# Optimization experiments

Measured on AMD Instinct MI355X. Metric: run time of the kernel, lower is better.

Reference implementation:

```python
import jax, jax.numpy as jnp
import numpy as np

C = 512
H = 8
P = 64
B = 4
N = 1024


def setup_inputs() -> dict:
    key = jax.random.key(0)
    ks = jax.random.split(key, 12)
    s = 0.02
    return {
        "tokens": jax.random.normal(ks[0], (B, N, C), dtype=jnp.float32),
        "pair_features": jax.random.normal(ks[1], (N, N, P), dtype=jnp.float32),
        "Wq": jax.random.normal(ks[2], (C, C), dtype=jnp.float32) * s,
        "bq": jnp.zeros((C,), dtype=jnp.float32),
        "Wk": jax.random.normal(ks[3], (C, C), dtype=jnp.float32) * s,
        "bk": jnp.zeros((C,), dtype=jnp.float32),
        "Wv": jax.random.normal(ks[4], (C, C), dtype=jnp.float32) * s,
        "bv": jnp.zeros((C,), dtype=jnp.float32),
        "Wo": jax.random.normal(ks[5], (C, C), dtype=jnp.float32) * s,
        "bo": jnp.zeros((C,), dtype=jnp.float32),
        "Wp": jax.random.normal(ks[6], (P, H), dtype=jnp.float32) * s,
    }


def reference(tokens, pair_features, Wq, bq, Wk, bk, Wv, bv, Wo, bo, Wp):
    b, n, c = tokens.shape
    h = H
    d = c // h
    scale = d ** -0.5
    # projections -> [b, h, n, d]
    q = (tokens @ Wq + bq).reshape(b, n, h, d).transpose(0, 2, 1, 3)
    k = (tokens @ Wk + bk).reshape(b, n, h, d).transpose(0, 2, 1, 3)
    v = (tokens @ Wv + bv).reshape(b, n, h, d).transpose(0, 2, 1, 3)
    # attention logits [b, h, n, n] with additive pair-derived bias [h, n, n]
    logits = jnp.einsum('bhnd,bhmd->bhnm', q, k) * scale
    pair_bias = jnp.einsum('nmp,ph->hnm', pair_features, Wp)
    logits = logits + pair_bias[None]
    attn = jax.nn.softmax(logits, axis=-1)  # dropout p=0.0 -> identity
    merged = jnp.einsum('bhnm,bhmd->bhnd', attn, v)
    merged = merged.transpose(0, 2, 1, 3).reshape(b, n, c)
    return merged @ Wo + bo
```

## Files before the change

### kernel.cpp

```cpp
#include <hip/hip_runtime.h>
#include <hip/hip_bf16.h>
#include <stdint.h>
#include <stddef.h>

typedef __bf16 bf16x8 __attribute__((ext_vector_type(8)));
typedef __bf16 bf16x4 __attribute__((ext_vector_type(4)));
typedef float  f32x4  __attribute__((ext_vector_type(4)));
typedef uint32_t __attribute__((address_space(3))) lds_u32;
typedef uint32_t __attribute__((address_space(1))) glob_u32;

#define QKV_BLOCKS 384
#define PAIR_BLOCKS 2048
#define NSPLIT 2
#define NITER  8
#define LOG2E 1.4426950408889634f

__global__ __launch_bounds__(256) void k1_kernel(
    const float* __restrict__ tokens, const float* __restrict__ pf,
    const float* __restrict__ Wq, const float* __restrict__ Wk,
    const float* __restrict__ Wv, const float* __restrict__ Wp,
    const float* __restrict__ bq, const float* __restrict__ bk,
    const float* __restrict__ bv,
    __bf16* __restrict__ qb, __bf16* __restrict__ kb, __bf16* __restrict__ vtb,
    __bf16* __restrict__ pbb) {
  __shared__ __align__(16) char smem_raw[37504];
  int bx = blockIdx.x, tid = threadIdx.x;
  if (bx < QKV_BLOCKS) {
    __bf16 (*As)[40] = (__bf16(*)[40])smem_raw;
    __bf16 (*Bs)[40] = (__bf16(*)[40])(smem_raw + 10240);
    float (*ftile)[133] = (float(*)[133])(smem_raw + 20480);
    const float qscale = 0.125f * LOG2E;
    int nb = bx % 12, mb = bx / 12;
    int m0 = mb * 128, n0 = nb * 128;
    int sel = n0 >> 9, cloc = n0 & 511;
    const float* W = sel == 0 ? Wq : sel == 1 ? Wk : Wv;
    int wave = tid >> 6, lane = tid & 63;
    int wm = (wave >> 1) * 64, wn = (wave & 1) * 64;
    int lg = lane >> 4, lr = lane & 15;
    f32x4 acc[4][4];
#pragma unroll
    for (int i = 0; i < 4; ++i)
#pragma unroll
      for (int j = 0; j < 4; ++j) acc[i][j] = (f32x4){0.f, 0.f, 0.f, 0.f};

    for (int k0 = 0; k0 < 512; k0 += 32) {
      __syncthreads();
#pragma unroll
      for (int i = 0; i < 2; ++i) {
        int cid = tid + i * 256;
        int row = cid >> 2, c8 = (cid & 3) * 8;
        const float* src = &tokens[(size_t)(m0 + row) * 512 + k0 + c8];
        f32x4 f0 = *(const f32x4*)src, f1 = *(const f32x4*)(src + 4);
        bf16x8 v;
#pragma unroll
        for (int u = 0; u < 4; ++u) { v[u] = (__bf16)f0[u]; v[u + 4] = (__bf16)f1[u]; }
        *(bf16x8*)&As[row][c8] = v;
      }
#pragma unroll
      for (int i = 0; i < 2; ++i) {
        int cid = tid + i * 256;
        int kk = cid >> 4, n8 = (cid & 15) * 8;
        const float* src = &W[(size_t)(k0 + kk) * 512 + cloc + n8];
        *(f32x4*)&ftile[kk][n8] = *(const f32x4*)src;
        *(f32x4*)&ftile[kk][n8 + 4] = *(const f32x4*)(src + 4);
      }
      __syncthreads();
#pragma unroll
      for (int i = 0; i < 2; ++i) {
        int cid = tid + i * 256;
        int n = cid >> 2, kk8 = (cid & 3) * 8;
        bf16x8 v;
#pragma unroll
        for (int u = 0; u < 8; ++u) v[u] = (__bf16)ftile[kk8 + u][n];
        *(bf16x8*)&Bs[n][kk8] = v;
      }
      __syncthreads();
      bf16x8 af[4], bfr[4];
#pragma unroll
      for (int i = 0; i < 4; ++i) {
        af[i]  = *(const bf16x8*)&As[wm + i * 16 + lr][lg * 8];
        bfr[i] = *(const bf16x8*)&Bs[wn + i * 16 + lr][lg * 8];
      }
#pragma unroll
      for (int i = 0; i < 4; ++i)
#pragma unroll
        for (int j = 0; j < 4; ++j)
          acc[i][j] = __builtin_amdgcn_mfma_f32_16x16x32_bf16(af[i], bfr[j], acc[i][j], 0, 0, 0);
    }
#pragma unroll
    for (int i = 0; i < 4; ++i)
#pragma unroll
      for (int j = 0; j < 4; ++j) {
        int grow0 = m0 + wm + i * 16 + lg * 4;
        int gcol = n0 + wn + j * 16 + lr;
        int gsel = gcol >> 9, c = gcol & 511;
        int hh = c >> 6, dd = c & 63;
        int b = grow0 >> 10, n = grow0 & 1023;
        if (gsel == 2) {
          float bias = bv[c];
          bf16x4 pack;
#pragma unroll
          for (int r = 0; r < 4; ++r) pack[r] = (__bf16)(acc[i][j][r] + bias);
          *(bf16x4*)&vtb[(((size_t)(b * 8 + hh)) * 64 + dd) * 1024 + n] = pack;
        } else if (gsel == 0) {
          float bias = bq[c];
#pragma unroll
          for (int r = 0; r < 4; ++r)
            qb[(((size_t)(b * 8 + hh)) * 1024 + n + r) * 64 + dd] = (__bf16)((acc[i][j][r] + bias) * qscale);
        } else {
          float bias = bk[c];
#pragma unroll
          for (int r = 0; r < 4; ++r)
            kb[(((size_t)(b * 8 + hh)) * 1024 + n + r) * 64 + dd] = (__bf16)(acc[i][j][r] + bias);
        }
      }
  } else {
    int pb = bx - QKV_BLOCKS;
    int wave = tid >> 6, lane = tid & 63;
    int lg = lane >> 4, lr = lane & 15;
    bf16x8 wfrag[2];
#pragma unroll
    for (int s = 0; s < 2; ++s)
#pragma unroll
      for (int j = 0; j < 8; ++j) {
        int p = s * 32 + lg * 8 + j;
        wfrag[s][j] = (lr < 8) ? (__bf16)Wp[p * 8 + lr] : (__bf16)0.f;
      }
    char* psbase = smem_raw + wave * 4096;
    int wbase = pb * 512 + wave * 128;
    int wrow_lo = lane >> 4;
    int wcol = lane & 15;
#pragma unroll 2
    for (int it = 0; it < 8; ++it) {
      int rowt = wbase + it * 16;
      const float* base = pf + (size_t)rowt * 64;
      f32x4 v[4];
#pragma unroll
      for (int j = 0; j < 4; ++j)
        v[j] = *(const f32x4*)(base + j * 256 + lane * 4);
      char* ps = psbase + (it & 1) * 2048;
#pragma unroll
      for (int j = 0; j < 4; ++j) {
        int jr = j * 4 + wrow_lo;
        bf16x4 b;
#pragma unroll
        for (int u = 0; u < 4; ++u) b[u] = (__bf16)v[j][u];
        int cbyte = ((((wcol >> 1) ^ (jr & 7)) << 4) | ((wcol & 1) << 3));
        *(bf16x4*)(ps + jr * 128 + cbyte) = b;
      }
      bf16x8 af[2];
#pragma unroll
      for (int s = 0; s < 2; ++s) {
        int cb = ((s * 4 + lg) ^ (lr & 7)) << 4;
        af[s] = *(const bf16x8*)(ps + lr * 128 + cb);
      }
      f32x4 acc = {0.f, 0.f, 0.f, 0.f};
      acc = __builtin_amdgcn_mfma_f32_16x16x32_bf16(af[0], wfrag[0], acc, 0, 0, 0);
      acc = __builtin_amdgcn_mfma_f32_16x16x32_bf16(af[1], wfrag[1], acc, 0, 0, 0);
      if (lr < 8) {
        bf16x4 pk;
#pragma unroll
        for (int r = 0; r < 4; ++r) pk[r] = (__bf16)(acc[r] * LOG2E);
        *(bf16x4*)&pbb[((size_t)lr << 20) + rowt + lg * 4] = pk;
      }
    }
  }
}

__device__ __forceinline__ bf16x8 swz_read(const __bf16* buf, int r, int k) {
  int chunk = (r << 3) | (k ^ (r & 7));
  return *(const bf16x8*)&buf[chunk * 8];
}

__global__ __launch_bounds__(256) void flash_kernel(const __bf16* __restrict__ qg,
                                                    const __bf16* __restrict__ kg,
                                                    const __bf16* __restrict__ vtg,
                                                    const __bf16* __restrict__ pbg,
                                                    float* __restrict__ po,
                                                    float2* __restrict__ ml) {
  __shared__ __align__(16) __bf16 kvs[2][2][64 * 64];
  __shared__ __bf16 pls[4][16][72];
  int bh = blockIdx.y, z = blockIdx.z, h = bh & 7;
  int q0 = blockIdx.x * 64;
  int tid = threadIdx.x, wave = tid >> 6, lane = tid & 63;
  int lg = lane >> 4, lr = lane & 15;
  const __bf16* qp = qg + (size_t)bh * 65536;
  const __bf16* kp = kg + (size_t)bh * 65536;
  const __bf16* vp = vtg + (size_t)bh * 65536;
  const __bf16* pbh = pbg + ((size_t)h << 20);
  int qw0 = q0 + wave * 16;
  int kb0 = z * NITER;

  auto stage = [&](int buf, int kb2) {
#pragma unroll
    for (int p = 0; p < 2; ++p) {
      int c = p * 256 + wave * 64 + lane;
      int r = c >> 3, kk = c & 7;
      int g = (c & ~7) | (kk ^ (r & 7));
      const __bf16* gk = kp + (size_t)kb2 * 4096 + g * 8;
      const __bf16* gv = vp + (size_t)(g >> 3) * 1024 + kb2 * 64 + (g & 7) * 8;
      __builtin_amdgcn_global_load_lds((const glob_u32*)gk,
          (lds_u32*)&kvs[buf][0][(size_t)(p * 256 + wave * 64) * 8], 16, 0, 0);
      __builtin_amdgcn_global_load_lds((const glob_u32*)gv,
          (lds_u32*)&kvs[buf][1][(size_t)(p * 256 + wave * 64) * 8], 16, 0, 0);
    }
  };

  bf16x8 qf[2];
#pragma unroll
  for (int c = 0; c < 2; ++c)
    qf[c] = *(const bf16x8*)&qp[(size_t)(qw0 + lr) * 64 + c * 32 + lg * 8];

  float mrow = -1e30f, lrow = 0.f;
  f32x4 of[4] = {};

  stage(0, kb0);
  __syncthreads();

#pragma unroll
  for (int t = 0; t < NITER; ++t) {
    int kb2 = kb0 + t;
    if (t + 1 < NITER) stage((t + 1) & 1, kb2 + 1);
    const __bf16* kbuf = &kvs[t & 1][0][0];
    const __bf16* vbuf = &kvs[t & 1][1][0];

    bf16x8 kf[4][2];
#pragma unroll
    for (int n = 0; n < 4; ++n)
#pragma unroll
      for (int c = 0; c < 2; ++c)
        kf[n][c] = swz_read(kbuf, n * 16 + lr, c * 4 + lg);

    f32x4 sv[4];
#pragma unroll
    for (int n = 0; n < 4; ++n) {
      bf16x4 bias = *(const bf16x4*)&pbh[(size_t)(qw0 + lr) * 1024 + kb2 * 64 + n * 16 + lg * 4];
      f32x4 cb;
#pragma unroll
      for (int r = 0; r < 4; ++r) cb[r] = (float)bias[r];
      cb = __builtin_amdgcn_mfma_f32_16x16x32_bf16(kf[n][0], qf[0], cb, 0, 0, 0);
      cb = __builtin_amdgcn_mfma_f32_16x16x32_bf16(kf[n][1], qf[1], cb, 0, 0, 0);
      sv[n] = cb;
    }

    float tm = -1e30f;
#pragma unroll
    for (int n = 0; n < 4; ++n)
#pragma unroll
      for (int r = 0; r < 4; ++r) tm = fmaxf(tm, sv[n][r]);
    tm = fmaxf(tm, __shfl_xor(tm, 16));
    tm = fmaxf(tm, __shfl_xor(tm, 32));
    float newm = fmaxf(mrow, tm);
    float fs = exp2f(mrow - newm);
    mrow = newm;
    float rs = 0.f;
#pragma unroll
    for (int n = 0; n < 4; ++n)
#pragma unroll
      for (int r = 0; r < 4; ++r) {
        float p = exp2f(sv[n][r] - newm);
        sv[n][r] = p;
        rs += p;
      }
    rs += __shfl_xor(rs, 16);
    rs += __shfl_xor(rs, 32);
    lrow = lrow * fs + rs;

#pragma unroll
    for (int n = 0; n < 4; ++n) {
      bf16x4 pk;
#pragma unroll
      for (int r = 0; r < 4; ++r) pk[r] = (__bf16)sv[n][r];
      *(bf16x4*)&pls[wave][lr][n * 16 + lg * 4] = pk;
    }

#pragma unroll
    for (int r = 0; r < 4; ++r) {
      float fsq = __shfl(fs, (lane & 48) | (lg * 4 + r));
#pragma unroll
      for (int dn = 0; dn < 4; ++dn) of[dn][r] *= fsq;
    }

    bf16x8 pa[2];
#pragma unroll
    for (int c = 0; c < 2; ++c)
      pa[c] = *(const bf16x8*)&pls[wave][lr][c * 32 + lg * 8];
    bf16x8 vf[4][2];
#pragma unroll
    for (int dn = 0; dn < 4; ++dn)
#pragma unroll
      for (int c = 0; c < 2; ++c)
        vf[dn][c] = swz_read(vbuf, dn * 16 + lr, c * 4 + lg);
#pragma unroll
    for (int dn = 0; dn < 4; ++dn) {
      of[dn] = __builtin_amdgcn_mfma_f32_16x16x32_bf16(pa[0], vf[dn][0], of[dn], 0, 0, 0);
      of[dn] = __builtin_amdgcn_mfma_f32_16x16x32_bf16(pa[1], vf[dn][1], of[dn], 0, 0, 0);
    }
    __syncthreads();
  }

  if (lg == 0)
    ml[(size_t)z * 32768 + bh * 1024 + qw0 + lr] = make_float2(mrow, lrow);
#pragma unroll
  for (int r = 0; r < 4; ++r) {
    int q = qw0 + lg * 4 + r;
#pragma unroll
    for (int dn = 0; dn < 4; ++dn)
      po[((size_t)z * 32768 + bh * 1024 + q) * 64 + dn * 16 + lr] = of[dn][r];
  }
}

__global__ __launch_bounds__(256) void combine_kernel(const float* __restrict__ po,
                                                      const float2* __restrict__ ml,
                                                      __bf16* __restrict__ merged) {
  int e = blockIdx.x * 256 + threadIdx.x;
  int row = e >> 5, d2 = (e & 31) * 2;
  int bh = row >> 10, q = row & 1023, b = bh >> 3, h = bh & 7;
  float2 s[NSPLIT];
  float M = -1e30f;
#pragma unroll
  for (int zz = 0; zz < NSPLIT; ++zz) {
    s[zz] = ml[(size_t)zz * 32768 + row];
    M = fmaxf(M, s[zz].x);
  }
  float L = 0.f, ox = 0.f, oy = 0.f;
#pragma unroll
  for (int zz = 0; zz < NSPLIT; ++zz) {
    float w = exp2f(s[zz].x - M);
    L += w * s[zz].y;
    float2 p = *(const float2*)&po[((size_t)zz * 32768 + row) * 64 + d2];
    ox += w * p.x;
    oy += w * p.y;
  }
  float inv = 1.f / L;
  __bf16 pr[2] = {(__bf16)(ox * inv), (__bf16)(oy * inv)};
  *(uint32_t*)&merged[((size_t)(b * 1024 + q)) * 512 + h * 64 + d2] = *(uint32_t*)pr;
}

__global__ __launch_bounds__(256) void out_gemm_kernel(const __bf16* __restrict__ A,
                                                       const float* __restrict__ Wo,
                                                       const float* __restrict__ bo,
                                                       float* __restrict__ out) {
  __shared__ __bf16 As[128][40];
  __shared__ __bf16 Bs[128][40];
  __shared__ float ftile[32][133];
  int m0 = blockIdx.y * 128, n0 = blockIdx.x * 128;
  int tid = threadIdx.x, wave = tid >> 6, lane = tid & 63;
  int wm = (wave >> 1) * 64, wn = (wave & 1) * 64, lg = lane >> 4, lr = lane & 15;
  f32x4 acc[4][4];
#pragma unroll
  for (int i = 0; i < 4; ++i)
#pragma unroll
    for (int j = 0; j < 4; ++j) acc[i][j] = (f32x4){0.f, 0.f, 0.f, 0.f};

  for (int k0 = 0; k0 < 512; k0 += 32) {
    __syncthreads();
#pragma unroll
    for (int i = 0; i < 2; ++i) {
      int cid = tid + i * 256;
      int row = cid >> 2, c8 = (cid & 3) * 8;
      *(bf16x8*)&As[row][c8] = *(const bf16x8*)&A[(size_t)(m0 + row) * 512 + k0 + c8];
    }
#pragma unroll
    for (int i = 0; i < 2; ++i) {
      int cid = tid + i * 256;
      int kk = cid >> 4, n8 = (cid & 15) * 8;
      const float* src = &Wo[(size_t)(k0 + kk) * 512 + n0 + n8];
      *(f32x4*)&ftile[kk][n8] = *(const f32x4*)src;
      *(f32x4*)&ftile[kk][n8 + 4] = *(const f32x4*)(src + 4);
    }
    __syncthreads();
#pragma unroll
    for (int i = 0; i < 2; ++i) {
      int cid = tid + i * 256;
      int n = cid >> 2, kk8 = (cid & 3) * 8;
      bf16x8 v;
#pragma unroll
      for (int u = 0; u < 8; ++u) v[u] = (__bf16)ftile[kk8 + u][n];
      *(bf16x8*)&Bs[n][kk8] = v;
    }
    __syncthreads();
    bf16x8 af[4], bfr[4];
#pragma unroll
    for (int i = 0; i < 4; ++i) {
      af[i]  = *(const bf16x8*)&As[wm + i * 16 + lr][lg * 8];
      bfr[i] = *(const bf16x8*)&Bs[wn + i * 16 + lr][lg * 8];
    }
#pragma unroll
    for (int i = 0; i < 4; ++i)
#pragma unroll
      for (int j = 0; j < 4; ++j)
        acc[i][j] = __builtin_amdgcn_mfma_f32_16x16x32_bf16(af[i], bfr[j], acc[i][j], 0, 0, 0);
  }
#pragma unroll
  for (int i = 0; i < 4; ++i)
#pragma unroll
    for (int j = 0; j < 4; ++j)
#pragma unroll
      for (int r = 0; r < 4; ++r) {
        int grow = m0 + wm + i * 16 + lg * 4 + r;
        int gcol = n0 + wn + j * 16 + lr;
        out[(size_t)grow * 512 + gcol] = acc[i][j][r] + bo[gcol];
      }
}

extern "C" void kernel_launch(void* const* d_in, const int* in_sizes, int n_in,
                              void* d_out, int out_size, void* d_ws, size_t ws_size,
                              hipStream_t stream) {
  const float* tokens = (const float*)d_in[0];
  const float* pf     = (const float*)d_in[1];
  const float* Wq     = (const float*)d_in[2];
  const float* bq     = (const float*)d_in[3];
  const float* Wk     = (const float*)d_in[4];
  const float* bk     = (const float*)d_in[5];
  const float* Wv     = (const float*)d_in[6];
  const float* bv     = (const float*)d_in[7];
  const float* Wo     = (const float*)d_in[8];
  const float* bo     = (const float*)d_in[9];
  const float* Wp     = (const float*)d_in[10];
  float* out = (float*)d_out;

  char* ws = (char*)d_ws;
  size_t off = 0;
  auto alloc = [&](size_t bytes) { char* p = ws + off; off += (bytes + 255) & ~(size_t)255; return p; };
  __bf16* qb     = (__bf16*)alloc((size_t)32 * 1024 * 64 * 2);
  __bf16* kb     = (__bf16*)alloc((size_t)32 * 1024 * 64 * 2);
  __bf16* vtb    = (__bf16*)alloc((size_t)32 * 64 * 1024 * 2);
  __bf16* pbb    = (__bf16*)alloc((size_t)8 * 1024 * 1024 * 2);
  __bf16* merged = (__bf16*)alloc((size_t)4096 * 512 * 2);
  float*  po     = (float*)alloc((size_t)NSPLIT * 32 * 1024 * 64 * 4);
  float2* ml     = (float2*)alloc((size_t)NSPLIT * 32 * 1024 * 8);

  k1_kernel<<<QKV_BLOCKS + PAIR_BLOCKS, 256, 0, stream>>>(
      tokens, pf, Wq, Wk, Wv, Wp, bq, bk, bv, qb, kb, vtb, pbb);
  flash_kernel<<<dim3(16, 32, NSPLIT), 256, 0, stream>>>(qb, kb, vtb, pbb, po, ml);
  combine_kernel<<<4096, 256, 0, stream>>>(po, ml, merged);
  out_gemm_kernel<<<dim3(4, 32), 256, 0, stream>>>(merged, Wo, bo, out);
}
```

Before: 137.9 us.

## Software-pipeline pair-bias loads, reorder k1 blocks, swizzle P tile in LDS

In k1, the pair-feature projection blocks are now dispatched first, ahead of the QKV GEMM blocks. Their 8-iteration loop is fully unrolled with a three-slot register prefetch, so global loads for iteration it+2 are in flight while iteration it computes. Separately, the flash kernel's per-wave P staging buffer drops its padded 72-wide rows for 64-wide rows with an XOR swizzle, aimed at avoiding LDS bank conflicts at lower shared-memory use. The extra prefetch slots add register pressure in the pair path.

Result: slower. 157.7 us (+14.4%).

```diff
diff --git a/kernel.cpp b/kernel.cpp
--- a/kernel.cpp
+++ b/kernel.cpp
@@ -25,12 +25,76 @@
     __bf16* __restrict__ pbb) {
   __shared__ __align__(16) char smem_raw[37504];
   int bx = blockIdx.x, tid = threadIdx.x;
-  if (bx < QKV_BLOCKS) {
+  if (bx < PAIR_BLOCKS) {
+    int wave = tid >> 6, lane = tid & 63;
+    int lg = lane >> 4, lr = lane & 15;
+    bf16x8 wfrag[2];
+#pragma unroll
+    for (int s = 0; s < 2; ++s)
+#pragma unroll
+      for (int j = 0; j < 8; ++j) {
+        int p = s * 32 + lg * 8 + j;
+        wfrag[s][j] = (lr < 8) ? (__bf16)Wp[p * 8 + lr] : (__bf16)0.f;
+      }
+    char* psbase = smem_raw + wave * 4096;
+    int wbase = bx * 512 + wave * 128;
+    int wrow_lo = lane >> 4;
+    int wcol = lane & 15;
+
+    f32x4 v[3][4];
+    auto PLOAD = [&](int it, int slot) {
+      const float* base = pf + (size_t)(wbase + it * 16) * 64;
+#pragma unroll
+      for (int j = 0; j < 4; ++j)
+        v[slot][j] = *(const f32x4*)(base + j * 256 + lane * 4);
+    };
+    auto PWLDS = [&](int it, int slot) {
+      char* ps = psbase + (it & 1) * 2048;
+#pragma unroll
+      for (int j = 0; j < 4; ++j) {
+        int jr = j * 4 + wrow_lo;
+        bf16x4 b;
+#pragma unroll
+        for (int u = 0; u < 4; ++u) b[u] = (__bf16)v[slot][j][u];
+        int cbyte = ((((wcol >> 1) ^ (jr & 7)) << 4) | ((wcol & 1) << 3));
+        *(bf16x4*)(ps + jr * 128 + cbyte) = b;
+      }
+    };
+    auto PCOMP = [&](int it) {
+      char* ps = psbase + (it & 1) * 2048;
+      bf16x8 af[2];
+#pragma unroll
+      for (int s = 0; s < 2; ++s) {
+        int cb = ((s * 4 + lg) ^ (lr & 7)) << 4;
+        af[s] = *(const bf16x8*)(ps + lr * 128 + cb);
+      }
+      f32x4 acc = {0.f, 0.f, 0.f, 0.f};
+      acc = __builtin_amdgcn_mfma_f32_16x16x32_bf16(af[0], wfrag[0], acc, 0, 0, 0);
+      acc = __builtin_amdgcn_mfma_f32_16x16x32_bf16(af[1], wfrag[1], acc, 0, 0, 0);
+      if (lr < 8) {
+        bf16x4 pk;
+#pragma unroll
+        for (int r = 0; r < 4; ++r) pk[r] = (__bf16)(acc[r] * LOG2E);
+        *(bf16x4*)&pbb[((size_t)lr << 20) + wbase + it * 16 + lg * 4] = pk;
+      }
+    };
+
+    PLOAD(0, 0);
+    PLOAD(1, 1);
+    PWLDS(0, 0);
+#pragma unroll
+    for (int it = 0; it < 8; ++it) {
+      if (it + 2 < 8) PLOAD(it + 2, (it + 2) % 3);
+      PCOMP(it);
+      if (it + 1 < 8) PWLDS(it + 1, (it + 1) % 3);
+    }
+  } else {
     __bf16 (*As)[40] = (__bf16(*)[40])smem_raw;
     __bf16 (*Bs)[40] = (__bf16(*)[40])(smem_raw + 10240);
     float (*ftile)[133] = (float(*)[133])(smem_raw + 20480);
     const float qscale = 0.125f * LOG2E;
-    int nb = bx % 12, mb = bx / 12;
+    int qid = bx - PAIR_BLOCKS;
+    int nb = qid % 12, mb = qid / 12;
     int m0 = mb * 128, n0 = nb * 128;
     int sel = n0 >> 9, cloc = n0 & 511;
     const float* W = sel == 0 ? Wq : sel == 1 ? Wk : Wv;
@@ -51,10 +115,10 @@
         int row = cid >> 2, c8 = (cid & 3) * 8;
         const float* src = &tokens[(size_t)(m0 + row) * 512 + k0 + c8];
         f32x4 f0 = *(const f32x4*)src, f1 = *(const f32x4*)(src + 4);
-        bf16x8 v;
-#pragma unroll
-        for (int u = 0; u < 4; ++u) { v[u] = (__bf16)f0[u]; v[u + 4] = (__bf16)f1[u]; }
-        *(bf16x8*)&As[row][c8] = v;
+        bf16x8 vv;
+#pragma unroll
+        for (int u = 0; u < 4; ++u) { vv[u] = (__bf16)f0[u]; vv[u + 4] = (__bf16)f1[u]; }
+        *(bf16x8*)&As[row][c8] = vv;
       }
 #pragma unroll
       for (int i = 0; i < 2; ++i) {
@@ -69,10 +133,10 @@
       for (int i = 0; i < 2; ++i) {
         int cid = tid + i * 256;
         int n = cid >> 2, kk8 = (cid & 3) * 8;
-        bf16x8 v;
-#pragma unroll
-        for (int u = 0; u < 8; ++u) v[u] = (__bf16)ftile[kk8 + u][n];
-        *(bf16x8*)&Bs[n][kk8] = v;
+        bf16x8 vv;
+#pragma unroll
+        for (int u = 0; u < 8; ++u) vv[u] = (__bf16)ftile[kk8 + u][n];
+        *(bf16x8*)&Bs[n][kk8] = vv;
       }
       __syncthreads();
       bf16x8 af[4], bfr[4];
@@ -114,56 +178,6 @@
             kb[(((size_t)(b * 8 + hh)) * 1024 + n + r) * 64 + dd] = (__bf16)(acc[i][j][r] + bias);
         }
       }
-  } else {
-    int pb = bx - QKV_BLOCKS;
-    int wave = tid >> 6, lane = tid & 63;
-    int lg = lane >> 4, lr = lane & 15;
-    bf16x8 wfrag[2];
-#pragma unroll
-    for (int s = 0; s < 2; ++s)
-#pragma unroll
-      for (int j = 0; j < 8; ++j) {
-        int p = s * 32 + lg * 8 + j;
-        wfrag[s][j] = (lr < 8) ? (__bf16)Wp[p * 8 + lr] : (__bf16)0.f;
-      }
-    char* psbase = smem_raw + wave * 4096;
-    int wbase = pb * 512 + wave * 128;
-    int wrow_lo = lane >> 4;
-    int wcol = lane & 15;
-#pragma unroll 2
-    for (int it = 0; it < 8; ++it) {
-      int rowt = wbase + it * 16;
-      const float* base = pf + (size_t)rowt * 64;
-      f32x4 v[4];
-#pragma unroll
-      for (int j = 0; j < 4; ++j)
-        v[j] = *(const f32x4*)(base + j * 256 + lane * 4);
-      char* ps = psbase + (it & 1) * 2048;
-#pragma unroll
-      for (int j = 0; j < 4; ++j) {
-        int jr = j * 4 + wrow_lo;
-        bf16x4 b;
-#pragma unroll
-        for (int u = 0; u < 4; ++u) b[u] = (__bf16)v[j][u];
-        int cbyte = ((((wcol >> 1) ^ (jr & 7)) << 4) | ((wcol & 1) << 3));
-        *(bf16x4*)(ps + jr * 128 + cbyte) = b;
-      }
-      bf16x8 af[2];
-#pragma unroll
-      for (int s = 0; s < 2; ++s) {
-        int cb = ((s * 4 + lg) ^ (lr & 7)) << 4;
-        af[s] = *(const bf16x8*)(ps + lr * 128 + cb);
-      }
-      f32x4 acc = {0.f, 0.f, 0.f, 0.f};
-      acc = __builtin_amdgcn_mfma_f32_16x16x32_bf16(af[0], wfrag[0], acc, 0, 0, 0);
-      acc = __builtin_amdgcn_mfma_f32_16x16x32_bf16(af[1], wfrag[1], acc, 0, 0, 0);
-      if (lr < 8) {
-        bf16x4 pk;
-#pragma unroll
-        for (int r = 0; r < 4; ++r) pk[r] = (__bf16)(acc[r] * LOG2E);
-        *(bf16x4*)&pbb[((size_t)lr << 20) + rowt + lg * 4] = pk;
-      }
-    }
   }
 }
 
@@ -179,7 +193,7 @@
                                                     float* __restrict__ po,
                                                     float2* __restrict__ ml) {
   __shared__ __align__(16) __bf16 kvs[2][2][64 * 64];
-  __shared__ __bf16 pls[4][16][72];
+  __shared__ __align__(16) __bf16 pls[4][16][64];
   int bh = blockIdx.y, z = blockIdx.z, h = bh & 7;
   int q0 = blockIdx.x * 64;
   int tid = threadIdx.x, wave = tid >> 6, lane = tid & 63;
@@ -190,6 +204,7 @@
   const __bf16* pbh = pbg + ((size_t)h << 20);
   int qw0 = q0 + wave * 16;
   int kb0 = z * NITER;
+  char* pwave = (char*)&pls[wave][0][0];
 
   auto stage = [&](int buf, int kb2) {
 #pragma unroll
@@ -271,7 +286,8 @@
       bf16x4 pk;
 #pragma unroll
       for (int r = 0; r < 4; ++r) pk[r] = (__bf16)sv[n][r];
-      *(bf16x4*)&pls[wave][lr][n * 16 + lg * 4] = pk;
+      int ch = ((n * 2 + (lg >> 1)) ^ (lr & 7));
+      *(bf16x4*)(pwave + lr * 128 + ch * 16 + (lg & 1) * 8) = pk;
     }
 
 #pragma unroll
@@ -283,8 +299,10 @@
 
     bf16x8 pa[2];
 #pragma unroll
-    for (int c = 0; c < 2; ++c)
-      pa[c] = *(const bf16x8*)&pls[wave][lr][c * 32 + lg * 8];
+    for (int c = 0; c < 2; ++c) {
+      int ch = ((c * 4 + lg) ^ (lr & 7));
+      pa[c] = *(const bf16x8*)(pwave + lr * 128 + ch * 16);
+    }
     bf16x8 vf[4][2];
 #pragma unroll
     for (int dn = 0; dn < 4; ++dn)
@@ -431,7 +449,7 @@
   float*  po     = (float*)alloc((size_t)NSPLIT * 32 * 1024 * 64 * 4);
   float2* ml     = (float2*)alloc((size_t)NSPLIT * 32 * 1024 * 8);
 
-  k1_kernel<<<QKV_BLOCKS + PAIR_BLOCKS, 256, 0, stream>>>(
+  k1_kernel<<<PAIR_BLOCKS + QKV_BLOCKS, 256, 0, stream>>>(
       tokens, pf, Wq, Wk, Wv, Wp, bq, bk, bv, qb, kb, vtb, pbb);
   flash_kernel<<<dim3(16, 32, NSPLIT), 256, 0, stream>>>(qb, kb, vtb, pbb, po, ml);
   combine_kernel<<<4096, 256, 0, stream>>>(po, ml, merged);
```
